# Optimization experiments

Measured on AMD Instinct MI355X. Metric: run time of the kernel, lower is better.

## Reference

```python
import jax, jax.numpy as jnp
import numpy as np

B, S, E = 8, 2048, 1024
H, DK = 128, 8  # embed_dim = H * DK; DK = n_wires per quantum head


def setup_inputs() -> dict:
    key = jax.random.key(0)
    k1, k2, k3, k4 = jax.random.split(key, 4)
    x = jax.random.normal(k1, (B, S, E), dtype=jnp.float32)
    theta = jax.random.normal(k2, (H, DK), dtype=jnp.float32)  # trainable RX angles per head/wire
    W = jax.random.normal(k3, (E, E), dtype=jnp.float32) * (1.0 / np.sqrt(E))
    b = jax.random.normal(k4, (E,), dtype=jnp.float32) * 0.01
    return {"x": x, "theta": theta, "W": W, "b": b}


def reference(x, theta, W, b):
    # Quantum circuit per token/head: RX(x_i) then RX(theta_i) on wire i starting
    # from |0...0>. Single-qubit RX gates compose: RX(a)RX(b)=RX(a+b), and
    # <Z> after RX(angle)|0> = cos(angle). So the MeasureAll(PauliZ) output is
    # cos(x_i + theta_i) elementwise -- fully vectorized over batch/seq/head/wire.
    Bx, Sx, Ex = x.shape
    Hx, dk = theta.shape
    xs = x.reshape(Bx, Sx, Hx, dk)            # [B,S,H,dk]
    head_out = jnp.cos(xs + theta[None, None])  # [B,S,H,dk]
    out = head_out.reshape(Bx, Sx, Ex)
    return out @ W.T + b                       # combine Linear
```

## Files before the change

kernel.cpp:

```cpp
#include <hip/hip_runtime.h>
#include <hip/hip_bf16.h>
#include <stdint.h>

#define M_DIM 16384
#define N_DIM 1024
#define K_DIM 1024

typedef __attribute__((ext_vector_type(8))) short short8;
typedef __attribute__((ext_vector_type(4))) float f32x4;

#define GLD_LDS(g, l) __builtin_amdgcn_global_load_lds( \
    (const __attribute__((address_space(1))) unsigned int*)(g), \
    (__attribute__((address_space(3))) unsigned int*)(l), 16, 0, 0)

__device__ __forceinline__ unsigned short f2bf(float f) {
  union { float f; unsigned int u; } v;
  v.f = f;
  unsigned int u = v.u + 0x7FFFu + ((v.u >> 16) & 1u);
  return (unsigned short)(u >> 16);
}

#define PREP_A_BLOCKS (M_DIM * K_DIM / (256 * 8))
#define PREP_W_BLOCKS (N_DIM * K_DIM / (256 * 8))
__global__ __launch_bounds__(256) void prep_all(const float* __restrict__ x,
                                                const float* __restrict__ theta,
                                                const float* __restrict__ W,
                                                unsigned short* __restrict__ A,
                                                unsigned short* __restrict__ Wb) {
  if (blockIdx.x < PREP_A_BLOCKS) {
    const long i = ((long)blockIdx.x * 256 + threadIdx.x) * 8;
    const int k = (int)(i & (K_DIM - 1));
    float4 x0 = *(const float4*)(x + i);
    float4 x1 = *(const float4*)(x + i + 4);
    float4 t0 = *(const float4*)(theta + k);
    float4 t1 = *(const float4*)(theta + k + 4);
    union { unsigned short s[8]; short8 v; } o;
    o.s[0] = f2bf(__cosf(x0.x + t0.x));
    o.s[1] = f2bf(__cosf(x0.y + t0.y));
    o.s[2] = f2bf(__cosf(x0.z + t0.z));
    o.s[3] = f2bf(__cosf(x0.w + t0.w));
    o.s[4] = f2bf(__cosf(x1.x + t1.x));
    o.s[5] = f2bf(__cosf(x1.y + t1.y));
    o.s[6] = f2bf(__cosf(x1.z + t1.z));
    o.s[7] = f2bf(__cosf(x1.w + t1.w));
    *(short8*)(A + i) = o.v;
  } else {
    const long i = ((long)(blockIdx.x - PREP_A_BLOCKS) * 256 + threadIdx.x) * 8;
    float4 w0 = *(const float4*)(W + i);
    float4 w1 = *(const float4*)(W + i + 4);
    union { unsigned short s[8]; short8 v; } o;
    o.s[0] = f2bf(w0.x); o.s[1] = f2bf(w0.y); o.s[2] = f2bf(w0.z); o.s[3] = f2bf(w0.w);
    o.s[4] = f2bf(w1.x); o.s[5] = f2bf(w1.y); o.s[6] = f2bf(w1.z); o.s[7] = f2bf(w1.w);
    *(short8*)(Wb + i) = o.v;
  }
}

__global__ __launch_bounds__(256) void gemm_bt(const unsigned short* __restrict__ A,
                                               const unsigned short* __restrict__ Bt,
                                               const float* __restrict__ bias,
                                               float* __restrict__ C) {
  constexpr int BM = 128, BN = 128, BK = 64;
  __shared__ unsigned short As[BM * BK];
  __shared__ unsigned short Bs[BN * BK];
  const int tid = threadIdx.x;

  const int L = blockIdx.y * 8 + blockIdx.x;
  const int bx = (L >> 3) & 7;
  const int by = (L & 7) * 16 + (L >> 6);
  const int m0 = by * BM;
  const int n0 = bx * BN;

  const int lane = tid & 63;
  const int wave = tid >> 6;
  const int wm = (wave >> 1) * 64;
  const int wn = (wave & 1) * 64;

  f32x4 acc[4][4] = {};

  const int srow = tid >> 3;
  const int scol = ((tid & 7) ^ (srow & 7)) * 8;
  const unsigned short* Ag = A + (long)(m0 + srow) * K_DIM + scol;
  const unsigned short* Bg = Bt + (long)(n0 + srow) * K_DIM + scol;
  unsigned short* Asd = As + tid * 8;
  unsigned short* Bsd = Bs + tid * 8;

  for (int k0 = 0; k0 < K_DIM; k0 += BK) {
    __syncthreads();
#pragma unroll
    for (int i = 0; i < 4; ++i)
      GLD_LDS(Ag + (long)i * 32 * K_DIM, Asd + i * 2048);
#pragma unroll
    for (int i = 0; i < 4; ++i)
      GLD_LDS(Bg + (long)i * 32 * K_DIM, Bsd + i * 2048);
    Ag += BK;
    Bg += BK;
    __syncthreads();

#pragma unroll
    for (int s = 0; s < 2; ++s) {
      const int kr = s * 32 + (lane >> 4) * 8;
      const int c = kr >> 3;
      short8 af[4], bf[4];
#pragma unroll
      for (int i = 0; i < 4; ++i) {
        const int r = wm + i * 16 + (lane & 15);
        af[i] = *(const short8*)(As + r * BK + (c ^ (r & 7)) * 8);
      }
#pragma unroll
      for (int j = 0; j < 4; ++j) {
        const int r = wn + j * 16 + (lane & 15);
        bf[j] = *(const short8*)(Bs + r * BK + (c ^ (r & 7)) * 8);
      }
#pragma unroll
      for (int i = 0; i < 4; ++i)
#pragma unroll
        for (int j = 0; j < 4; ++j)
          acc[i][j] = __builtin_amdgcn_mfma_f32_16x16x32_bf16(af[i], bf[j], acc[i][j], 0, 0, 0);
    }
  }

  const int cn = lane & 15;
  const int rq = (lane >> 4) * 4;
#pragma unroll
  for (int j = 0; j < 4; ++j) {
    const int n = n0 + wn + j * 16 + cn;
    const float bv = bias[n];
#pragma unroll
    for (int i = 0; i < 4; ++i) {
      const long mb = (long)(m0 + wm + i * 16 + rq) * N_DIM + n;
#pragma unroll
      for (int r = 0; r < 4; ++r)
        C[mb + (long)r * N_DIM] = acc[i][j][r] + bv;
    }
  }
}

extern "C" void kernel_launch(void* const* d_in, const int* in_sizes, int n_in,
                              void* d_out, int out_size, void* d_ws, size_t ws_size,
                              hipStream_t stream) {
  const float* x = (const float*)d_in[0];
  const float* theta = (const float*)d_in[1];
  const float* W = (const float*)d_in[2];
  const float* b = (const float*)d_in[3];
  float* out = (float*)d_out;

  unsigned short* Abf = (unsigned short*)d_ws;
  unsigned short* Wbf = Abf + (size_t)M_DIM * K_DIM;

  hipLaunchKernelGGL(prep_all, dim3(PREP_A_BLOCKS + PREP_W_BLOCKS), dim3(256), 0,
                     stream, x, theta, W, Abf, Wbf);
  hipLaunchKernelGGL(gemm_bt, dim3(N_DIM / 128, M_DIM / 128), dim3(256), 0, stream,
                     Abf, Wbf, b, out);
}
```

Measured before the change: 153.9 us.

## Switch GEMM to 32x32x16 MFMA and restructure prep kernel access pattern

The GEMM inner loop now uses 32x32x16 bf16 MFMA instructions with a 2x2 tile of 16-wide accumulators per wave, in place of 4x4 tiles of 16x16x32. This halves the LDS fragment reads per MFMA and uses the larger matrix instruction, which should raise compute density. The prep kernel also changes each thread's work from 8 contiguous elements to two strided float4 chunks, with theta loaded once per thread. The epilogue is rewritten to match the 32x32 output layout.

Result: slower. 157.5 us (+2.4%).

```diff
diff --git a/kernel.cpp b/kernel.cpp
--- a/kernel.cpp
+++ b/kernel.cpp
@@ -7,7 +7,7 @@
 #define K_DIM 1024
 
 typedef __attribute__((ext_vector_type(8))) short short8;
-typedef __attribute__((ext_vector_type(4))) float f32x4;
+typedef __attribute__((ext_vector_type(16))) float f32x16;
 
 #define GLD_LDS(g, l) __builtin_amdgcn_global_load_lds( \
     (const __attribute__((address_space(1))) unsigned int*)(g), \
@@ -20,38 +20,41 @@
   return (unsigned short)(u >> 16);
 }
 
-#define PREP_A_BLOCKS (M_DIM * K_DIM / (256 * 8))
-#define PREP_W_BLOCKS (N_DIM * K_DIM / (256 * 8))
+#define PREP_A_BLOCKS (M_DIM * K_DIM / 2048)
+#define PREP_W_BLOCKS (N_DIM * K_DIM / 2048)
 __global__ __launch_bounds__(256) void prep_all(const float* __restrict__ x,
                                                 const float* __restrict__ theta,
                                                 const float* __restrict__ W,
                                                 unsigned short* __restrict__ A,
                                                 unsigned short* __restrict__ Wb) {
+  const int tid = threadIdx.x;
   if (blockIdx.x < PREP_A_BLOCKS) {
-    const long i = ((long)blockIdx.x * 256 + threadIdx.x) * 8;
-    const int k = (int)(i & (K_DIM - 1));
-    float4 x0 = *(const float4*)(x + i);
-    float4 x1 = *(const float4*)(x + i + 4);
-    float4 t0 = *(const float4*)(theta + k);
-    float4 t1 = *(const float4*)(theta + k + 4);
-    union { unsigned short s[8]; short8 v; } o;
-    o.s[0] = f2bf(__cosf(x0.x + t0.x));
-    o.s[1] = f2bf(__cosf(x0.y + t0.y));
-    o.s[2] = f2bf(__cosf(x0.z + t0.z));
-    o.s[3] = f2bf(__cosf(x0.w + t0.w));
-    o.s[4] = f2bf(__cosf(x1.x + t1.x));
-    o.s[5] = f2bf(__cosf(x1.y + t1.y));
-    o.s[6] = f2bf(__cosf(x1.z + t1.z));
-    o.s[7] = f2bf(__cosf(x1.w + t1.w));
-    *(short8*)(A + i) = o.v;
+    const long base = (long)blockIdx.x * 2048;
+    const float4 t = *(const float4*)(theta + tid * 4);
+#pragma unroll
+    for (int p = 0; p < 2; ++p) {
+      const long i = base + p * 1024 + tid * 4;
+      const float4 xv = *(const float4*)(x + i);
+      ushort4 o;
+      o.x = f2bf(__cosf(xv.x + t.x));
+      o.y = f2bf(__cosf(xv.y + t.y));
+      o.z = f2bf(__cosf(xv.z + t.z));
+      o.w = f2bf(__cosf(xv.w + t.w));
+      *(ushort4*)(A + i) = o;
+    }
   } else {
-    const long i = ((long)(blockIdx.x - PREP_A_BLOCKS) * 256 + threadIdx.x) * 8;
-    float4 w0 = *(const float4*)(W + i);
-    float4 w1 = *(const float4*)(W + i + 4);
-    union { unsigned short s[8]; short8 v; } o;
-    o.s[0] = f2bf(w0.x); o.s[1] = f2bf(w0.y); o.s[2] = f2bf(w0.z); o.s[3] = f2bf(w0.w);
-    o.s[4] = f2bf(w1.x); o.s[5] = f2bf(w1.y); o.s[6] = f2bf(w1.z); o.s[7] = f2bf(w1.w);
-    *(short8*)(Wb + i) = o.v;
+    const long base = (long)(blockIdx.x - PREP_A_BLOCKS) * 2048;
+#pragma unroll
+    for (int p = 0; p < 2; ++p) {
+      const long i = base + p * 1024 + tid * 4;
+      const float4 wv = *(const float4*)(W + i);
+      ushort4 o;
+      o.x = f2bf(wv.x);
+      o.y = f2bf(wv.y);
+      o.z = f2bf(wv.z);
+      o.w = f2bf(wv.w);
+      *(ushort4*)(Wb + i) = o;
+    }
   }
 }
 
@@ -75,7 +78,7 @@
   const int wm = (wave >> 1) * 64;
   const int wn = (wave & 1) * 64;
 
-  f32x4 acc[4][4] = {};
+  f32x16 acc[2][2] = {};
 
   const int srow = tid >> 3;
   const int scol = ((tid & 7) ^ (srow & 7)) * 8;
@@ -83,6 +86,9 @@
   const unsigned short* Bg = Bt + (long)(n0 + srow) * K_DIM + scol;
   unsigned short* Asd = As + tid * 8;
   unsigned short* Bsd = Bs + tid * 8;
+
+  const int fr = lane & 31;
+  const int kh = (lane >> 5) * 8;
 
   for (int k0 = 0; k0 < K_DIM; k0 += BK) {
     __syncthreads();
@@ -97,40 +103,41 @@
     __syncthreads();
 
 #pragma unroll
-    for (int s = 0; s < 2; ++s) {
-      const int kr = s * 32 + (lane >> 4) * 8;
-      const int c = kr >> 3;
-      short8 af[4], bf[4];
+    for (int ks = 0; ks < 4; ++ks) {
+      const int c = (ks * 16 + kh) >> 3;
+      short8 af[2], bf[2];
 #pragma unroll
-      for (int i = 0; i < 4; ++i) {
-        const int r = wm + i * 16 + (lane & 15);
+      for (int i = 0; i < 2; ++i) {
+        const int r = wm + i * 32 + fr;
         af[i] = *(const short8*)(As + r * BK + (c ^ (r & 7)) * 8);
       }
 #pragma unroll
-      for (int j = 0; j < 4; ++j) {
-        const int r = wn + j * 16 + (lane & 15);
+      for (int j = 0; j < 2; ++j) {
+        const int r = wn + j * 32 + fr;
         bf[j] = *(const short8*)(Bs + r * BK + (c ^ (r & 7)) * 8);
       }
 #pragma unroll
-      for (int i = 0; i < 4; ++i)
+      for (int i = 0; i < 2; ++i)
 #pragma unroll
-        for (int j = 0; j < 4; ++j)
-          acc[i][j] = __builtin_amdgcn_mfma_f32_16x16x32_bf16(af[i], bf[j], acc[i][j], 0, 0, 0);
+        for (int j = 0; j < 2; ++j)
+          acc[i][j] = __builtin_amdgcn_mfma_f32_32x32x16_bf16(af[i], bf[j], acc[i][j], 0, 0, 0);
     }
   }
 
-  const int cn = lane & 15;
-  const int rq = (lane >> 4) * 4;
+  const int cn = lane & 31;
+  const int rbase = (lane >> 5) * 4;
 #pragma unroll
-  for (int j = 0; j < 4; ++j) {
-    const int n = n0 + wn + j * 16 + cn;
+  for (int j = 0; j < 2; ++j) {
+    const int n = n0 + wn + j * 32 + cn;
     const float bv = bias[n];
 #pragma unroll
-    for (int i = 0; i < 4; ++i) {
-      const long mb = (long)(m0 + wm + i * 16 + rq) * N_DIM + n;
+    for (int i = 0; i < 2; ++i) {
+      const long mrow = (long)(m0 + wm + i * 32 + rbase);
 #pragma unroll
-      for (int r = 0; r < 4; ++r)
-        C[mb + (long)r * N_DIM] = acc[i][j][r] + bv;
+      for (int r = 0; r < 16; ++r) {
+        const long row = mrow + (r & 3) + 8 * (r >> 2);
+        C[row * N_DIM + n] = acc[i][j][r] + bv;
+      }
     }
   }
 }
```

## Fuse cosine activation and bf16 conversion into GEMM A-tile loading

Applied to the files above, without the earlier changes.

Removes the separate pass that writes cos(x+theta) as a bf16 A matrix. The GEMM kernel now reads fp32 x directly, computes the cosine, converts to bf16 and stores the result into LDS, while W is still pre-converted by a smaller kernel. This avoids writing and re-reading a 32 MB intermediate. In exchange each A tile is recomputed by all 8 N-blocks, which means 8x redundant fp32 x reads (64 MB per column block, mostly from cache) and extra transcendental work inside the GEMM main loop. The loads also move from async global-to-LDS copies to synchronous register loads.

Result: slower. 192.6 us (+25.1%).

```diff
diff --git a/kernel.cpp b/kernel.cpp
--- a/kernel.cpp
+++ b/kernel.cpp
@@ -20,45 +20,29 @@
   return (unsigned short)(u >> 16);
 }
 
-#define PREP_A_BLOCKS (M_DIM * K_DIM / (256 * 8))
-#define PREP_W_BLOCKS (N_DIM * K_DIM / (256 * 8))
-__global__ __launch_bounds__(256) void prep_all(const float* __restrict__ x,
-                                                const float* __restrict__ theta,
-                                                const float* __restrict__ W,
-                                                unsigned short* __restrict__ A,
-                                                unsigned short* __restrict__ Wb) {
-  if (blockIdx.x < PREP_A_BLOCKS) {
-    const long i = ((long)blockIdx.x * 256 + threadIdx.x) * 8;
-    const int k = (int)(i & (K_DIM - 1));
-    float4 x0 = *(const float4*)(x + i);
-    float4 x1 = *(const float4*)(x + i + 4);
-    float4 t0 = *(const float4*)(theta + k);
-    float4 t1 = *(const float4*)(theta + k + 4);
-    union { unsigned short s[8]; short8 v; } o;
-    o.s[0] = f2bf(__cosf(x0.x + t0.x));
-    o.s[1] = f2bf(__cosf(x0.y + t0.y));
-    o.s[2] = f2bf(__cosf(x0.z + t0.z));
-    o.s[3] = f2bf(__cosf(x0.w + t0.w));
-    o.s[4] = f2bf(__cosf(x1.x + t1.x));
-    o.s[5] = f2bf(__cosf(x1.y + t1.y));
-    o.s[6] = f2bf(__cosf(x1.z + t1.z));
-    o.s[7] = f2bf(__cosf(x1.w + t1.w));
-    *(short8*)(A + i) = o.v;
-  } else {
-    const long i = ((long)(blockIdx.x - PREP_A_BLOCKS) * 256 + threadIdx.x) * 8;
-    float4 w0 = *(const float4*)(W + i);
-    float4 w1 = *(const float4*)(W + i + 4);
-    union { unsigned short s[8]; short8 v; } o;
-    o.s[0] = f2bf(w0.x); o.s[1] = f2bf(w0.y); o.s[2] = f2bf(w0.z); o.s[3] = f2bf(w0.w);
-    o.s[4] = f2bf(w1.x); o.s[5] = f2bf(w1.y); o.s[6] = f2bf(w1.z); o.s[7] = f2bf(w1.w);
-    *(short8*)(Wb + i) = o.v;
+#define PREP_W_BLOCKS (N_DIM * K_DIM / 2048)
+__global__ __launch_bounds__(256) void prep_w(const float* __restrict__ W,
+                                              unsigned short* __restrict__ Wb) {
+  const int tid = threadIdx.x;
+  const long base = (long)blockIdx.x * 2048;
+#pragma unroll
+  for (int p = 0; p < 2; ++p) {
+    const long i = base + p * 1024 + tid * 4;
+    const float4 wv = *(const float4*)(W + i);
+    ushort4 o;
+    o.x = f2bf(wv.x);
+    o.y = f2bf(wv.y);
+    o.z = f2bf(wv.z);
+    o.w = f2bf(wv.w);
+    *(ushort4*)(Wb + i) = o;
   }
 }
 
-__global__ __launch_bounds__(256) void gemm_bt(const unsigned short* __restrict__ A,
-                                               const unsigned short* __restrict__ Bt,
-                                               const float* __restrict__ bias,
-                                               float* __restrict__ C) {
+__global__ __launch_bounds__(256) void gemm_fused(const float* __restrict__ x,
+                                                  const float* __restrict__ theta,
+                                                  const unsigned short* __restrict__ Bt,
+                                                  const float* __restrict__ bias,
+                                                  float* __restrict__ C) {
   constexpr int BM = 128, BN = 128, BK = 64;
   __shared__ unsigned short As[BM * BK];
   __shared__ unsigned short Bs[BN * BK];
@@ -78,22 +62,38 @@
   f32x4 acc[4][4] = {};
 
   const int srow = tid >> 3;
-  const int scol = ((tid & 7) ^ (srow & 7)) * 8;
-  const unsigned short* Ag = A + (long)(m0 + srow) * K_DIM + scol;
-  const unsigned short* Bg = Bt + (long)(n0 + srow) * K_DIM + scol;
+  const int scol8 = (tid & 7) ^ (srow & 7);
+  const unsigned short* Bg = Bt + (long)(n0 + srow) * K_DIM + scol8 * 8;
+  unsigned short* Bsd = Bs + tid * 8;
+  const float* xg = x + (long)(m0 + srow) * K_DIM + scol8 * 8;
   unsigned short* Asd = As + tid * 8;
-  unsigned short* Bsd = Bs + tid * 8;
 
   for (int k0 = 0; k0 < K_DIM; k0 += BK) {
     __syncthreads();
 #pragma unroll
     for (int i = 0; i < 4; ++i)
-      GLD_LDS(Ag + (long)i * 32 * K_DIM, Asd + i * 2048);
+      GLD_LDS(Bg + (long)i * 32 * K_DIM, Bsd + i * 2048);
+    Bg += BK;
+
+    const int kc = k0 + scol8 * 8;
+    const float4 t0 = *(const float4*)(theta + kc);
+    const float4 t1 = *(const float4*)(theta + kc + 4);
 #pragma unroll
-    for (int i = 0; i < 4; ++i)
-      GLD_LDS(Bg + (long)i * 32 * K_DIM, Bsd + i * 2048);
-    Ag += BK;
-    Bg += BK;
+    for (int i = 0; i < 4; ++i) {
+      const float* xp = xg + (long)i * 32 * K_DIM + k0;
+      const float4 x0 = *(const float4*)(xp);
+      const float4 x1 = *(const float4*)(xp + 4);
+      union { unsigned short s[8]; short8 v; } o;
+      o.s[0] = f2bf(__cosf(x0.x + t0.x));
+      o.s[1] = f2bf(__cosf(x0.y + t0.y));
+      o.s[2] = f2bf(__cosf(x0.z + t0.z));
+      o.s[3] = f2bf(__cosf(x0.w + t0.w));
+      o.s[4] = f2bf(__cosf(x1.x + t1.x));
+      o.s[5] = f2bf(__cosf(x1.y + t1.y));
+      o.s[6] = f2bf(__cosf(x1.z + t1.z));
+      o.s[7] = f2bf(__cosf(x1.w + t1.w));
+      *(short8*)(Asd + i * 2048) = o.v;
+    }
     __syncthreads();
 
 #pragma unroll
@@ -104,12 +104,12 @@
 #pragma unroll
       for (int i = 0; i < 4; ++i) {
         const int r = wm + i * 16 + (lane & 15);
-        af[i] = *(const short8*)(As + r * BK + (c ^ (r & 7)) * 8);
+        af[i] = *(const short8*)(As + r * BK + ((c ^ (r & 7)) * 8));
       }
 #pragma unroll
       for (int j = 0; j < 4; ++j) {
         const int r = wn + j * 16 + (lane & 15);
-        bf[j] = *(const short8*)(Bs + r * BK + (c ^ (r & 7)) * 8);
+        bf[j] = *(const short8*)(Bs + r * BK + ((c ^ (r & 7)) * 8));
       }
 #pragma unroll
       for (int i = 0; i < 4; ++i)
@@ -144,11 +144,9 @@
   const float* b = (const float*)d_in[3];
   float* out = (float*)d_out;
 
-  unsigned short* Abf = (unsigned short*)d_ws;
-  unsigned short* Wbf = Abf + (size_t)M_DIM * K_DIM;
+  unsigned short* Wbf = (unsigned short*)d_ws;
 
-  hipLaunchKernelGGL(prep_all, dim3(PREP_A_BLOCKS + PREP_W_BLOCKS), dim3(256), 0,
-                     stream, x, theta, W, Abf, Wbf);
-  hipLaunchKernelGGL(gemm_bt, dim3(N_DIM / 128, M_DIM / 128), dim3(256), 0, stream,
-                     Abf, Wbf, b, out);
+  hipLaunchKernelGGL(prep_w, dim3(PREP_W_BLOCKS), dim3(256), 0, stream, W, Wbf);
+  hipLaunchKernelGGL(gemm_fused, dim3(N_DIM / 128, M_DIM / 128), dim3(256), 0, stream,
+                     x, theta, Wbf, b, out);
 }
```
